# Kernel tuning notes

Measured on AMD Instinct MI355X. Metric: run time of the kernel, lower is better.

The kernel has to match this reference:

```python
import jax, jax.numpy as jnp
import numpy as np

N = 50000
E = 800000
IN_C, HID, OUT_C, HEADS = 128, 32, 64, 4
NEG_SLOPE = 0.2


def setup_inputs() -> dict:
    key = jax.random.key(0)
    ks = jax.random.split(key, 10)
    x = jax.random.normal(ks[0], (N, IN_C), dtype=jnp.float32)
    edge_index = jax.random.randint(ks[1], (2, E), 0, N, dtype=jnp.int64)
    s = 0.05
    W1 = jax.random.normal(ks[2], (IN_C, HID), dtype=jnp.float32) * s
    b1 = jnp.zeros((HID,), dtype=jnp.float32)
    Wg = jax.random.normal(ks[3], (HID, HEADS * HID), dtype=jnp.float32) * s
    ag_src = jax.random.normal(ks[4], (HEADS, HID), dtype=jnp.float32) * s
    ag_dst = jax.random.normal(ks[5], (HEADS, HID), dtype=jnp.float32) * s
    bg = jnp.zeros((HID,), dtype=jnp.float32)
    W2 = jax.random.normal(ks[6], (HID, OUT_C), dtype=jnp.float32) * s
    b2 = jnp.zeros((OUT_C,), dtype=jnp.float32)
    return {"x": x, "edge_index": edge_index, "W1": W1, "b1": b1,
            "Wg": Wg, "ag_src": ag_src, "ag_dst": ag_dst, "bg": bg,
            "W2": W2, "b2": b2}


def _add_self_loops(edge_index, n):
    loop = jnp.arange(n, dtype=edge_index.dtype)
    return jnp.concatenate([edge_index, jnp.stack([loop, loop])], axis=1)


def _gcn(x, src, dst, W, b, n):
    # PyG GCNConv: symmetric normalization with self-loops, scatter-add
    xw = x @ W  # [N, F]
    deg = jnp.zeros((n,), xw.dtype).at[dst].add(1.0)  # in-degree incl self-loops
    dinv = jax.lax.rsqrt(deg)
    norm = dinv[src] * dinv[dst]  # [E']
    msg = xw[src] * norm[:, None]  # [E', F]
    out = jax.ops.segment_sum(msg, dst, num_segments=n)
    return out + b


def _gat(x, src, dst, Wg, a_src, a_dst, b, n):
    # PyG GATConv, concat=False (mean over heads), leaky_relu slope 0.2
    h = (x @ Wg).reshape(n, HEADS, HID)  # [N, H, D]
    al_s = jnp.einsum('nhd,hd->nh', h, a_src)  # [N, H]
    al_d = jnp.einsum('nhd,hd->nh', h, a_dst)
    logits = jax.nn.leaky_relu(al_s[src] + al_d[dst], NEG_SLOPE)  # [E', H]
    # segment softmax over incoming edges of each dst node
    m = jax.ops.segment_max(logits, dst, num_segments=n)
    e = jnp.exp(logits - m[dst])
    denom = jax.ops.segment_sum(e, dst, num_segments=n)
    alpha = e / denom[dst]  # [E', H]
    msg = h[src] * alpha[:, :, None]  # [E', H, D]
    out = jax.ops.segment_sum(msg, dst, num_segments=n)  # [N, H, D]
    return out.mean(axis=1) + b


def reference(x, edge_index, W1, b1, Wg, ag_src, ag_dst, bg, W2, b2):
    ei = _add_self_loops(edge_index, N)
    src, dst = ei[0], ei[1]
    h = jax.nn.relu(_gcn(x, src, dst, W1, b1, N))
    h = jax.nn.relu(_gat(h, src, dst, Wg, ag_src, ag_dst, bg, N))
    return _gcn(h, src, dst, W2, b2, N)
```

## Files before the change

kernel.cpp:

```cpp
#include <hip/hip_runtime.h>
#include <hip/hip_bf16.h>

#define N_NODES 50000
#define N_EDGES 800000
#define IN_C 128
#define HID 32
#define OUT_C 64
#define HEADS 4
#define NEG_SLOPE 0.2f

#define MAXDEG 64
#define SC_BLOCKS 2048
#define SC_G (SC_BLOCKS * 256)
#define N_PASS 4
#define PASS_W ((N_NODES + N_PASS - 1) / N_PASS)

typedef unsigned int uint32;
typedef unsigned short ushort16;
typedef __attribute__((ext_vector_type(8))) short bf16x8;
typedef __attribute__((ext_vector_type(4))) float f32x4;

__device__ __forceinline__ float bf_lo(uint32 u) { return __uint_as_float(u << 16); }
__device__ __forceinline__ float bf_hi(uint32 u) { return __uint_as_float(u & 0xffff0000u); }
__device__ __forceinline__ uint32 f2bf(float f) {
    uint32 u = __float_as_uint(f);
    return (u + 0x7fffu + ((u >> 16) & 1u)) >> 16;
}
__device__ __forceinline__ uint32 pack_bf2(float a, float b) {
    return f2bf(a) | (f2bf(b) << 16);
}

__global__ __launch_bounds__(256) void k_scatter(const int* __restrict__ ei,
                                                 int* __restrict__ ncnt,
                                                 ushort16* __restrict__ srcs_pad,
                                                 const float* __restrict__ Wg,
                                                 const float* __restrict__ ags,
                                                 const float* __restrict__ agd,
                                                 float* __restrict__ wals,
                                                 float* __restrict__ wald,
                                                 const float* __restrict__ W2,
                                                 uint32* __restrict__ wgB,
                                                 uint32* __restrict__ w2B) {
    int t = threadIdx.x;
    int gid = blockIdx.x * 256 + t;
    int s0 = 0, d0 = -1, s1 = 0, d1 = -1;
    if (gid < N_EDGES)        { s0 = ei[gid];        d0 = ei[N_EDGES + gid]; }
    if (gid + SC_G < N_EDGES) { s1 = ei[gid + SC_G]; d1 = ei[N_EDGES + gid + SC_G]; }
#pragma unroll
    for (int p = 0; p < N_PASS; p++) {
        int lo = p * PASS_W, hi = lo + PASS_W;
        if (d0 >= lo && d0 < hi) {
            int pos = atomicAdd(&ncnt[d0], 1);
            if (pos < MAXDEG) srcs_pad[(d0 << 6) + pos] = (ushort16)s0;
        }
        if (d1 >= lo && d1 < hi) {
            int pos = atomicAdd(&ncnt[d1], 1);
            if (pos < MAXDEG) srcs_pad[(d1 << 6) + pos] = (ushort16)s1;
        }
        __syncthreads();
    }
    if (blockIdx.x == 0) {
        {
            int c = t & 127;
            int h = c >> 5, k = c & 31;
            const float* a = (t < 128) ? ags : agd;
            float acc = 0.f;
#pragma unroll
            for (int d = 0; d < 32; d++) acc += Wg[k * 128 + h * 32 + d] * a[h * 32 + d];
            if (t < 128) wals[c] = acc; else wald[c] = acc;
        }
        for (int i = t; i < 2048; i += 256) {
            int tile = i >> 8;
            int T = tile >> 2, kt = tile & 3;
            int r = i & 255;
            int L = r >> 2, di = r & 3;
            int k0 = kt * 32 + (L >> 4) * 8 + 2 * di;
            int k1 = k0 + 1;
            int n = T * 16 + (L & 15);
            float a = Wg[(k0 & 31) * 128 + (k0 >> 5) * 32 + n];
            float b = Wg[(k1 & 31) * 128 + (k1 >> 5) * 32 + n];
            wgB[i] = pack_bf2(a, b);
        }
        for (int i = t; i < 1024; i += 256) {
            int T = i >> 8;
            int r = i & 255;
            int L = r >> 2, di = r & 3;
            int k0 = (L >> 4) * 8 + 2 * di;
            int n = T * 16 + (L & 15);
            w2B[i] = pack_bf2(W2[k0 * 64 + n], W2[(k0 + 1) * 64 + n]);
        }
    }
}

__global__ __launch_bounds__(256) void k_gemm1(const float* __restrict__ x,
                                               const float* __restrict__ W1,
                                               const int* __restrict__ ncnt,
                                               uint32* __restrict__ xw1) {
    __shared__ float wl[IN_C * HID];
    __shared__ float xl[8 * IN_C];
    int t = threadIdx.x;
    for (int i = t; i < IN_C * HID; i += 256) {
        int k = i >> 5, f = i & 31;
        wl[(k >> 1) * 64 + f * 2 + (k & 1)] = W1[i];
    }
    int nb = blockIdx.x * 8;
    const float4* x4 = (const float4*)(x + (size_t)nb * IN_C);
    ((float4*)xl)[t] = x4[t];
    __syncthreads();
    int g = t >> 5, f = t & 31;
    const float2* xr = (const float2*)(xl + g * IN_C);
    const float2* wp = (const float2*)wl;
    float acc = 0.f;
#pragma unroll 16
    for (int k2 = 0; k2 < 64; k2++) {
        float2 xv = xr[k2];
        float2 wv = wp[k2 * 32 + f];
        acc += xv.x * wv.x + xv.y * wv.y;
    }
    float v = acc * rsqrtf((float)(ncnt[nb + g] + 1));
    float vn = __shfl_xor(v, 1, 64);
    if ((f & 1) == 0) xw1[(size_t)(nb + g) * 16 + (f >> 1)] = pack_bf2(v, vn);
}

__global__ __launch_bounds__(256) void k_gather1(const uint32* __restrict__ xw1,
                                                 const int* __restrict__ ncnt,
                                                 const ushort16* __restrict__ srcs_pad,
                                                 const float* __restrict__ b1,
                                                 const float* __restrict__ wals,
                                                 const float* __restrict__ wald,
                                                 char* __restrict__ recH,
                                                 float* __restrict__ als,
                                                 float* __restrict__ ald) {
    int t = threadIdx.x;
    int l16 = t & 15;
    int es = l16 >> 2;
    int q  = l16 & 3;
    int n = blockIdx.x * 16 + (t >> 4);
    int deg = ncnt[n];
    float a0 = 0.f, a1 = 0.f, a2 = 0.f, a3 = 0.f;
    float a4 = 0.f, a5 = 0.f, a6 = 0.f, a7 = 0.f;
#pragma unroll 2
    for (int jb = 0; jb <= deg; jb += 4) {
        int je = jb + es;
        if (je <= deg) {
            int sidx = (je < deg) ? (int)srcs_pad[(n << 6) + je] : n;
            uint4 u = *(const uint4*)((const char*)xw1 + ((uint32)sidx << 6) + q * 16);
            a0 += bf_lo(u.x); a1 += bf_hi(u.x);
            a2 += bf_lo(u.y); a3 += bf_hi(u.y);
            a4 += bf_lo(u.z); a5 += bf_hi(u.z);
            a6 += bf_lo(u.w); a7 += bf_hi(u.w);
        }
    }
#define RED_ES(v) v += __shfl_xor(v, 4, 64); v += __shfl_xor(v, 8, 64);
    RED_ES(a0) RED_ES(a1) RED_ES(a2) RED_ES(a3)
    RED_ES(a4) RED_ES(a5) RED_ES(a6) RED_ES(a7)
#undef RED_ES
    float dn = rsqrtf((float)(deg + 1));
    float4 bA = ((const float4*)b1)[2 * q];
    float4 bB = ((const float4*)b1)[2 * q + 1];
    float v0 = a0 * dn + bA.x, v1 = a1 * dn + bA.y;
    float v2 = a2 * dn + bA.z, v3 = a3 * dn + bA.w;
    float v4 = a4 * dn + bB.x, v5 = a5 * dn + bB.y;
    float v6 = a6 * dn + bB.z, v7 = a7 * dn + bB.w;
    v0 = v0 > 0.f ? v0 : 0.f; v1 = v1 > 0.f ? v1 : 0.f;
    v2 = v2 > 0.f ? v2 : 0.f; v3 = v3 > 0.f ? v3 : 0.f;
    v4 = v4 > 0.f ? v4 : 0.f; v5 = v5 > 0.f ? v5 : 0.f;
    v6 = v6 > 0.f ? v6 : 0.f; v7 = v7 > 0.f ? v7 : 0.f;
    if (es == 0) {
        uint4 w;
        w.x = pack_bf2(v0, v1); w.y = pack_bf2(v2, v3);
        w.z = pack_bf2(v4, v5); w.w = pack_bf2(v6, v7);
        *(uint4*)(recH + ((uint32)n << 6) + q * 16) = w;
    }
    float ps[4], pd[4];
#pragma unroll
    for (int h = 0; h < 4; h++) {
        const float4* wa = (const float4*)(wals + h * 32 + 8 * q);
        float4 wv0 = wa[0], wv1 = wa[1];
        ps[h] = v0 * wv0.x + v1 * wv0.y + v2 * wv0.z + v3 * wv0.w
              + v4 * wv1.x + v5 * wv1.y + v6 * wv1.z + v7 * wv1.w;
        const float4* wb = (const float4*)(wald + h * 32 + 8 * q);
        float4 uv0 = wb[0], uv1 = wb[1];
        pd[h] = v0 * uv0.x + v1 * uv0.y + v2 * uv0.z + v3 * uv0.w
              + v4 * uv1.x + v5 * uv1.y + v6 * uv1.z + v7 * uv1.w;
    }
#pragma unroll
    for (int h = 0; h < 4; h++) {
        ps[h] += __shfl_xor(ps[h], 1, 64); ps[h] += __shfl_xor(ps[h], 2, 64);
        pd[h] += __shfl_xor(pd[h], 1, 64); pd[h] += __shfl_xor(pd[h], 2, 64);
    }
    if (l16 == 0) {
        ((float4*)als)[n] = make_float4(ps[0], ps[1], ps[2], ps[3]);
        ((float4*)ald)[n] = make_float4(pd[0], pd[1], pd[2], pd[3]);
    }
}

__global__ __launch_bounds__(512) void k_gat_agg(const char* __restrict__ recH,
                                                 const float* __restrict__ als,
                                                 const float* __restrict__ ald,
                                                 const int* __restrict__ ncnt,
                                                 const ushort16* __restrict__ srcs_pad,
                                                 const uint32* __restrict__ wgB,
                                                 const float* __restrict__ bg,
                                                 uint32* __restrict__ h2s) {
    __shared__ __align__(16) uint32 gl[16][64];
    int t = threadIdx.x;
    int l32 = t & 31;
    int g8 = t >> 5;
    int n = blockIdx.x * 16 + g8;
    int es = l32 >> 3;
    int q  = l32 & 7;
    int deg = ncnt[n];
    float4 dv = ((const float4*)ald)[n];

    float g00 = 0.f, g01 = 0.f, g02 = 0.f, g03 = 0.f;
    float g10 = 0.f, g11 = 0.f, g12 = 0.f, g13 = 0.f;
    float g20 = 0.f, g21 = 0.f, g22 = 0.f, g23 = 0.f;
    float g30 = 0.f, g31 = 0.f, g32 = 0.f, g33 = 0.f;
    float ss0 = 0.f, ss1 = 0.f, ss2 = 0.f, ss3 = 0.f;

#pragma unroll 2
    for (int jb = 0; jb <= deg; jb += 4) {
        int je = jb + es;
        if (je <= deg) {
            int sidx = (je < deg) ? (int)srcs_pad[(n << 6) + je] : n;
            float4 ev = ((const float4*)als)[sidx];
            uint2 u = *(const uint2*)(recH + ((uint32)sidx << 6) + q * 8);
            float f0 = bf_lo(u.x), f1 = bf_hi(u.x);
            float f2 = bf_lo(u.y), f3 = bf_hi(u.y);
            float tt, w;
            tt = ev.x + dv.x; w = __expf(fmaxf(tt, NEG_SLOPE * tt));
            ss0 += w; g00 += w * f0; g01 += w * f1; g02 += w * f2; g03 += w * f3;
            tt = ev.y + dv.y; w = __expf(fmaxf(tt, NEG_SLOPE * tt));
            ss1 += w; g10 += w * f0; g11 += w * f1; g12 += w * f2; g13 += w * f3;
            tt = ev.z + dv.z; w = __expf(fmaxf(tt, NEG_SLOPE * tt));
            ss2 += w; g20 += w * f0; g21 += w * f1; g22 += w * f2; g23 += w * f3;
            tt = ev.w + dv.w; w = __expf(fmaxf(tt, NEG_SLOPE * tt));
            ss3 += w; g30 += w * f0; g31 += w * f1; g32 += w * f2; g33 += w * f3;
        }
    }
#define RED_ES(v) v += __shfl_xor(v, 8, 64); v += __shfl_xor(v, 16, 64);
    RED_ES(ss0) RED_ES(ss1) RED_ES(ss2) RED_ES(ss3)
    RED_ES(g00) RED_ES(g01) RED_ES(g02) RED_ES(g03)
    RED_ES(g10) RED_ES(g11) RED_ES(g12) RED_ES(g13)
    RED_ES(g20) RED_ES(g21) RED_ES(g22) RED_ES(g23)
    RED_ES(g30) RED_ES(g31) RED_ES(g32) RED_ES(g33)
#undef RED_ES
    float i0 = 0.25f / ss0, i1 = 0.25f / ss1, i2 = 0.25f / ss2, i3 = 0.25f / ss3;
    if (es == 0) {
        uint2 w;
        w.x = pack_bf2(g00 * i0, g01 * i0); w.y = pack_bf2(g02 * i0, g03 * i0);
        *(uint2*)&gl[g8][0 * 16 + 2 * q] = w;
        w.x = pack_bf2(g10 * i1, g11 * i1); w.y = pack_bf2(g12 * i1, g13 * i1);
        *(uint2*)&gl[g8][1 * 16 + 2 * q] = w;
        w.x = pack_bf2(g20 * i2, g21 * i2); w.y = pack_bf2(g22 * i2, g23 * i2);
        *(uint2*)&gl[g8][2 * 16 + 2 * q] = w;
        w.x = pack_bf2(g30 * i3, g31 * i3); w.y = pack_bf2(g32 * i3, g33 * i3);
        *(uint2*)&gl[g8][3 * 16 + 2 * q] = w;
    }
    __syncthreads();
    if (t < 64) {
        int L = t;
        int mA = L & 15;
        int quad = L >> 4;
        int nbase = blockIdx.x * 16;
        float dns[4];
#pragma unroll
        for (int r = 0; r < 4; r++)
            dns[r] = rsqrtf((float)(ncnt[nbase + quad * 4 + r] + 1));
#pragma unroll
        for (int T = 0; T < 2; T++) {
            f32x4 acc = {0.f, 0.f, 0.f, 0.f};
#pragma unroll
            for (int kt = 0; kt < 4; kt++) {
                bf16x8 af = *(const bf16x8*)&gl[mA][kt * 16 + quad * 4];
                bf16x8 bf = *(const bf16x8*)(wgB + (size_t)((T * 4 + kt) * 64 + L) * 4);
                acc = __builtin_amdgcn_mfma_f32_16x16x32_bf16(af, bf, acc, 0, 0, 0);
            }
            int d = T * 16 + (L & 15);
            float bgd = bg[d];
#pragma unroll
            for (int r = 0; r < 4; r++) {
                int node = nbase + quad * 4 + r;
                float v = acc[r] + bgd;
                v = v > 0.f ? v : 0.f;
                v *= dns[r];
                float vn = __shfl_xor(v, 1, 64);
                if ((d & 1) == 0)
                    h2s[(size_t)node * 16 + (d >> 1)] = pack_bf2(v, vn);
            }
        }
    }
}

__global__ __launch_bounds__(256) void k_gather2(const uint32* __restrict__ h2s,
                                                 const int* __restrict__ ncnt,
                                                 const ushort16* __restrict__ srcs_pad,
                                                 const uint32* __restrict__ w2B,
                                                 const float* __restrict__ b2,
                                                 float* __restrict__ out) {
    __shared__ __align__(16) uint32 gbf[16][16];
    int t = threadIdx.x;
    int l16 = t & 15;
    int es = l16 >> 2;
    int q  = l16 & 3;
    int g16 = t >> 4;
    int n = blockIdx.x * 16 + g16;
    int deg = ncnt[n];
    float a0 = 0.f, a1 = 0.f, a2 = 0.f, a3 = 0.f;
    float a4 = 0.f, a5 = 0.f, a6 = 0.f, a7 = 0.f;
#pragma unroll 2
    for (int jb = 0; jb <= deg; jb += 4) {
        int je = jb + es;
        if (je <= deg) {
            int sidx = (je < deg) ? (int)srcs_pad[(n << 6) + je] : n;
            uint4 u = *(const uint4*)((const char*)h2s + ((uint32)sidx << 6) + q * 16);
            a0 += bf_lo(u.x); a1 += bf_hi(u.x);
            a2 += bf_lo(u.y); a3 += bf_hi(u.y);
            a4 += bf_lo(u.z); a5 += bf_hi(u.z);
            a6 += bf_lo(u.w); a7 += bf_hi(u.w);
        }
    }
#define RED_ES(v) v += __shfl_xor(v, 4, 64); v += __shfl_xor(v, 8, 64);
    RED_ES(a0) RED_ES(a1) RED_ES(a2) RED_ES(a3)
    RED_ES(a4) RED_ES(a5) RED_ES(a6) RED_ES(a7)
#undef RED_ES
    if (es == 0) {
        uint4 w;
        w.x = pack_bf2(a0, a1); w.y = pack_bf2(a2, a3);
        w.z = pack_bf2(a4, a5); w.w = pack_bf2(a6, a7);
        *(uint4*)&gbf[g16][4 * q] = w;
    }
    __syncthreads();
    if (t < 64) {
        int L = t;
        int quad = L >> 4;
        int nbase = blockIdx.x * 16;
        float dns[4];
#pragma unroll
        for (int r = 0; r < 4; r++)
            dns[r] = rsqrtf((float)(ncnt[nbase + quad * 4 + r] + 1));
        bf16x8 af = *(const bf16x8*)&gbf[L & 15][quad * 4];
#pragma unroll
        for (int T = 0; T < 4; T++) {
            bf16x8 bf = *(const bf16x8*)(w2B + (size_t)(T * 64 + L) * 4);
            f32x4 acc = {0.f, 0.f, 0.f, 0.f};
            acc = __builtin_amdgcn_mfma_f32_16x16x32_bf16(af, bf, acc, 0, 0, 0);
            int d = T * 16 + (L & 15);
            float b2d = b2[d];
#pragma unroll
            for (int r = 0; r < 4; r++) {
                int node = nbase + quad * 4 + r;
                out[(size_t)node * OUT_C + d] = acc[r] * dns[r] + b2d;
            }
        }
    }
}

extern "C" void kernel_launch(void* const* d_in, const int* in_sizes, int n_in,
                              void* d_out, int out_size, void* d_ws, size_t ws_size,
                              hipStream_t stream) {
    const float* x   = (const float*)d_in[0];
    const int*   ei  = (const int*)d_in[1];
    const float* W1  = (const float*)d_in[2];
    const float* b1  = (const float*)d_in[3];
    const float* Wg  = (const float*)d_in[4];
    const float* ags = (const float*)d_in[5];
    const float* agd = (const float*)d_in[6];
    const float* bg  = (const float*)d_in[7];
    const float* W2  = (const float*)d_in[8];
    const float* b2  = (const float*)d_in[9];
    float* out = (float*)d_out;

    char* p = (char*)d_ws;
    auto alloc = [&](size_t bytes) -> void* {
        void* r = (void*)p;
        p += (bytes + 255) & ~(size_t)255;
        return r;
    };
    int*      ncnt     = (int*)    alloc((size_t)N_NODES * 4);
    ushort16* srcs_pad = (ushort16*)alloc((size_t)N_NODES * MAXDEG * 2);
    uint32*   xw1      = (uint32*) alloc((size_t)N_NODES * 16 * 4);
    char*     recH     = (char*)   alloc((size_t)N_NODES * 64);
    float*    als      = (float*)  alloc((size_t)N_NODES * 4 * 4);
    float*    ald      = (float*)  alloc((size_t)N_NODES * 4 * 4);
    float*    wals     = (float*)  alloc(128 * 4);
    float*    wald     = (float*)  alloc(128 * 4);
    uint32*   wgB      = (uint32*) alloc(2048 * 4);
    uint32*   w2B      = (uint32*) alloc(1024 * 4);
    uint32*   h2s      = (uint32*) alloc((size_t)N_NODES * 16 * 4);

    hipMemsetAsync(ncnt, 0, (size_t)N_NODES * 4, stream);

    k_scatter<<<SC_BLOCKS, 256, 0, stream>>>(
        ei, ncnt, srcs_pad, Wg, ags, agd, wals, wald, W2, wgB, w2B);

    k_gemm1<<<N_NODES / 8, 256, 0, stream>>>(x, W1, ncnt, xw1);

    k_gather1<<<N_NODES / 16, 256, 0, stream>>>(xw1, ncnt, srcs_pad, b1,
                                                wals, wald, recH, als, ald);

    k_gat_agg<<<N_NODES / 16, 512, 0, stream>>>(recH, als, ald, ncnt, srcs_pad,
                                                wgB, bg, h2s);

    k_gather2<<<N_NODES / 16, 256, 0, stream>>>(h2s, ncnt, srcs_pad, w2B, b2, out);
}
```

Baseline: 222.9 us.

## Partition edge scatter by destination range across blocks instead of per-block passes

Replaces the in-block multi-pass scatter (4 passes with __syncthreads) with a scheme where each block handles one of 8 destination-node partitions over a contiguous edge chunk. Blocks sharing a partition cluster their atomics and padded-list writes into a smaller node range, which is meant to improve L2 locality of the atomics and remove the intra-block barriers. In exchange each edge's destination is read by 8 blocks, increasing index read traffic.

```diff
diff --git a/kernel.cpp b/kernel.cpp
--- a/kernel.cpp
+++ b/kernel.cpp
@@ -10,10 +10,11 @@
 #define NEG_SLOPE 0.2f
 
 #define MAXDEG 64
+#define N_PART 8
+#define PART_W ((N_NODES + N_PART - 1) / N_PART)
 #define SC_BLOCKS 2048
-#define SC_G (SC_BLOCKS * 256)
-#define N_PASS 4
-#define PASS_W ((N_NODES + N_PASS - 1) / N_PASS)
+#define RANKS (SC_BLOCKS / N_PART)
+#define EPB ((N_EDGES + RANKS - 1) / RANKS)
 
 typedef unsigned int uint32;
 typedef unsigned short ushort16;
@@ -42,22 +43,18 @@
                                                  uint32* __restrict__ wgB,
                                                  uint32* __restrict__ w2B) {
     int t = threadIdx.x;
-    int gid = blockIdx.x * 256 + t;
-    int s0 = 0, d0 = -1, s1 = 0, d1 = -1;
-    if (gid < N_EDGES)        { s0 = ei[gid];        d0 = ei[N_EDGES + gid]; }
-    if (gid + SC_G < N_EDGES) { s1 = ei[gid + SC_G]; d1 = ei[N_EDGES + gid + SC_G]; }
-#pragma unroll
-    for (int p = 0; p < N_PASS; p++) {
-        int lo = p * PASS_W, hi = lo + PASS_W;
-        if (d0 >= lo && d0 < hi) {
-            int pos = atomicAdd(&ncnt[d0], 1);
-            if (pos < MAXDEG) srcs_pad[(d0 << 6) + pos] = (ushort16)s0;
-        }
-        if (d1 >= lo && d1 < hi) {
-            int pos = atomicAdd(&ncnt[d1], 1);
-            if (pos < MAXDEG) srcs_pad[(d1 << 6) + pos] = (ushort16)s1;
-        }
-        __syncthreads();
+    int part = blockIdx.x & (N_PART - 1);
+    int rank = blockIdx.x >> 3;
+    int lo = part * PART_W;
+    int e0 = rank * EPB;
+    int e1 = e0 + EPB; if (e1 > N_EDGES) e1 = N_EDGES;
+    for (int e = e0 + t; e < e1; e += 256) {
+        int d = ei[N_EDGES + e];
+        if ((uint32)(d - lo) < (uint32)PART_W) {
+            int s = ei[e];
+            int pos = atomicAdd(&ncnt[d], 1);
+            if (pos < MAXDEG) srcs_pad[(d << 6) + pos] = (ushort16)s;
+        }
     }
     if (blockIdx.x == 0) {
         {
```

Result: no change. 223.4 us (+0.3%).
